# Optimization experiments

Measured on AMD Instinct MI355X. Metric: run time of the kernel, lower is better.

## Reference

```python
import jax, jax.numpy as jnp
import numpy as np

B, N, D, H = 4, 2048, 1024, 16
HD = D // H


def setup_inputs() -> dict:
    key = jax.random.key(0)
    ks = jax.random.split(key, 9)
    s = 1.0 / np.sqrt(D)
    return {
        "x": jax.random.normal(ks[0], (B, N, D), jnp.float32),
        "Wq": jax.random.normal(ks[1], (D, D), jnp.float32) * s,
        "bq": jnp.zeros((D,), jnp.float32),
        "Wk": jax.random.normal(ks[2], (D, D), jnp.float32) * s,
        "bk": jnp.zeros((D,), jnp.float32),
        "Wv": jax.random.normal(ks[3], (D, D), jnp.float32) * s,
        "bv": jnp.zeros((D,), jnp.float32),
        "Wo": jax.random.normal(ks[4], (D, D), jnp.float32) * s,
        "bo": jnp.zeros((D,), jnp.float32),
    }


def reference(x, Wq, bq, Wk, bk, Wv, bv, Wo, bo):
    Bx, Nx, Dx = x.shape
    q = x @ Wq + bq  # [B,N,D]
    k = x @ Wk + bk
    v = x @ Wv + bv
    # split heads -> [B,H,N,hd]
    q = q.reshape(Bx, Nx, H, HD).transpose(0, 2, 1, 3)
    k = k.reshape(Bx, Nx, H, HD).transpose(0, 2, 1, 3)
    v = v.reshape(Bx, Nx, H, HD).transpose(0, 2, 1, 3)
    q = q / jnp.sqrt(jnp.asarray(HD, q.dtype))
    scores = jnp.einsum("bhqd,bhkd->bhqk", q, k)
    # causal mask: additive -1e9 strictly above diagonal (matches torch.triu diag=1)
    mask = jnp.triu(jnp.full((Nx, Nx), -1e9, dtype=scores.dtype), k=1)
    probs = jax.nn.softmax(scores + mask, axis=-1)
    out = jnp.einsum("bhqk,bhkd->bhqd", probs, v)  # [B,H,N,hd]
    out = out.transpose(0, 2, 1, 3).reshape(Bx, Nx, Dx)  # concat heads
    return out @ Wo + bo
```

## Files before the change

### kernel.cpp

```cpp
#include <hip/hip_runtime.h>
#include <hip/hip_bf16.h>


#define BB 4
#define NN 2048
#define DD 1024
#define HH 16
#define HD 64
#define MM (BB * NN)

typedef __bf16 bf16;
typedef __bf16 bf16x8 __attribute__((ext_vector_type(8)));
typedef float f32x4 __attribute__((ext_vector_type(4)));

__device__ __forceinline__ void async_copy16(bf16* lds, const bf16* g) {
    __builtin_amdgcn_global_load_lds(
        (const __attribute__((address_space(1))) void*)g,
        (__attribute__((address_space(3))) void*)lds, 16, 0, 0);
}

__global__ void convert_x(const float* __restrict__ x, bf16* __restrict__ xb) {
    int i = (blockIdx.x * 256 + threadIdx.x) * 4;
    float4 v = *(const float4*)&x[i];
    xb[i + 0] = (bf16)v.x;
    xb[i + 1] = (bf16)v.y;
    xb[i + 2] = (bf16)v.z;
    xb[i + 3] = (bf16)v.w;
}

__global__ void transpose_w4(const float* __restrict__ W0, const float* __restrict__ W1,
                             const float* __restrict__ W2, const float* __restrict__ W3,
                             bf16* __restrict__ Wt) {
    __shared__ float tile[32][33];
    const float* W = (blockIdx.z == 0) ? W0 : (blockIdx.z == 1) ? W1
                    : (blockIdx.z == 2) ? W2 : W3;
    bf16* out = Wt + (size_t)blockIdx.z * DD * DD;
    int tx = threadIdx.x, ty = threadIdx.y;
    int x0 = blockIdx.x * 32, y0 = blockIdx.y * 32;
#pragma unroll
    for (int i = 0; i < 32; i += 8)
        tile[ty + i][tx] = W[(size_t)(y0 + ty + i) * DD + x0 + tx];
    __syncthreads();
#pragma unroll
    for (int i = 0; i < 32; i += 8)
        out[(size_t)(x0 + ty + i) * DD + y0 + tx] = (bf16)tile[tx][ty + i];
}

template <int MODE>
__global__ __launch_bounds__(256) void gemm_bt(
    const bf16* __restrict__ A, const bf16* __restrict__ Wt,
    const float* __restrict__ b0, const float* __restrict__ b1,
    const float* __restrict__ b2, void* __restrict__ out0,
    void* __restrict__ out1, void* __restrict__ out2) {
    const int K = DD;
    __shared__ __align__(16) bf16 As[128 * 32];
    __shared__ __align__(16) bf16 Bs[128 * 32];
    __shared__ __align__(16) bf16 Cs[MODE == 0 ? 128 * 136 : 1];

    int m0 = blockIdx.x * 128;
    int n0 = blockIdx.y * 128;

    const bf16* Wz;
    const float* bias;
    void* out;
    float scale = 1.0f;
    int z = 0;
    if (MODE == 0) {
        z = blockIdx.z;
        Wz = Wt + (size_t)z * DD * DD;
        bias = (z == 0) ? b0 : ((z == 1) ? b1 : b2);
        out = (z == 0) ? out0 : ((z == 1) ? out1 : out2);
        if (z == 0) scale = 0.125f * 1.44269504f;
    } else {
        Wz = Wt; bias = b0; out = out0;
    }

    int tid = threadIdx.x;
    int w = tid >> 6, lane = tid & 63;
    int wm = w >> 1, wn = w & 1;
    int quad = lane >> 4, l16 = lane & 15;

    f32x4 acc[4][4];
#pragma unroll
    for (int i = 0; i < 4; i++)
#pragma unroll
        for (int j = 0; j < 4; j++) acc[i][j] = (f32x4){0.f, 0.f, 0.f, 0.f};

    for (int k0 = 0; k0 < K; k0 += 32) {
        __syncthreads();
#pragma unroll
        for (int j = 0; j < 2; j++) {
            int c = j * 256 + w * 64 + lane;
            int row = c >> 2, kk = (c & 3) * 8;
            async_copy16(&As[c * 8], &A[(size_t)(m0 + row) * K + k0 + kk]);
            async_copy16(&Bs[c * 8], &Wz[(size_t)(n0 + row) * K + k0 + kk]);
        }
        __syncthreads();

        bf16x8 af[4], bfm[4];
#pragma unroll
        for (int i = 0; i < 4; i++) {
            af[i] = *(const bf16x8*)&As[(wm * 64 + i * 16 + l16) * 32 + quad * 8];
            bfm[i] = *(const bf16x8*)&Bs[(wn * 64 + i * 16 + l16) * 32 + quad * 8];
        }
#pragma unroll
        for (int i = 0; i < 4; i++)
#pragma unroll
            for (int j = 0; j < 4; j++)
                acc[i][j] = __builtin_amdgcn_mfma_f32_16x16x32_bf16(
                    af[i], bfm[j], acc[i][j], 0, 0, 0);
    }

    if (MODE == 0) {
#pragma unroll
        for (int j = 0; j < 4; j++) {
            int nl = wn * 64 + j * 16 + l16;
            float bv = bias[n0 + nl];
#pragma unroll
            for (int i = 0; i < 4; i++) {
#pragma unroll
                for (int r = 0; r < 4; r++) {
                    int ml = wm * 64 + i * 16 + quad * 4 + r;
                    bf16 v = (bf16)((acc[i][j][r] + bv) * scale);
                    if (z == 2) Cs[nl * 136 + ml] = v;
                    else        Cs[ml * 136 + nl] = v;
                }
            }
        }
        __syncthreads();

        int bidx = m0 >> 11;
        int tok0 = m0 & (NN - 1);
        int hh0 = n0 >> 6;
        if (z != 2) {
#pragma unroll
            for (int hf = 0; hf < 2; hf++) {
                bf16* base = (bf16*)out + ((size_t)(bidx * HH + hh0 + hf) * NN + tok0) * HD;
#pragma unroll
                for (int k = 0; k < 4; k++) {
                    int f = k * 2048 + tid * 8;
                    int tok = f >> 6, hd = f & 63;
                    *(bf16x8*)&base[f] = *(const bf16x8*)&Cs[tok * 136 + hf * 64 + hd];
                }
            }
        } else {
#pragma unroll
            for (int hf = 0; hf < 2; hf++) {
#pragma unroll
                for (int k = 0; k < 4; k++) {
                    int hd = k * 16 + (tid >> 4);
                    int tk = (tid & 15) * 8;
                    bf16* dst = (bf16*)out +
                        ((size_t)(bidx * HH + hh0 + hf) * HD + hd) * NN + tok0 + tk;
                    *(bf16x8*)dst = *(const bf16x8*)&Cs[(hf * 64 + hd) * 136 + tk];
                }
            }
        }
    } else {
#pragma unroll
        for (int j = 0; j < 4; j++) {
            int n = n0 + wn * 64 + j * 16 + l16;
            float bv = bias[n];
#pragma unroll
            for (int i = 0; i < 4; i++) {
                int mrow = m0 + wm * 64 + i * 16 + quad * 4;
#pragma unroll
                for (int r = 0; r < 4; r++)
                    ((float*)out)[(size_t)(mrow + r) * DD + n] = acc[i][j][r] + bv;
            }
        }
    }
}

__global__ __launch_bounds__(256) void flash_attn(
    const bf16* __restrict__ Q, const bf16* __restrict__ Kg,
    const bf16* __restrict__ Vt_g, bf16* __restrict__ Oc) {
    __shared__ __align__(16) bf16 Ks[128 * 72];
    __shared__ __align__(16) bf16 Vs[64 * 136];
    __shared__ __align__(16) bf16 Ps[128 * 136];

    int bh = blockIdx.y;
    int b = bh >> 4, h = bh & 15;
    int tid = threadIdx.x;
    int w = tid >> 6, lane = tid & 63;
    int quad = lane >> 4, l16 = lane & 15;

    const bf16* Qb = Q + (size_t)bh * NN * HD;
    const bf16* Kb = Kg + (size_t)bh * NN * HD;
    const bf16* Vtb = Vt_g + (size_t)bh * HD * NN;

    bf16x8 ones;
#pragma unroll
    for (int i = 0; i < 8; i++) ones[i] = (bf16)1.0f;

    int kr[4], kc[4], vd[4], vk[4];
#pragma unroll
    for (int j = 0; j < 4; j++) {
        int c = j * 256 + tid;
        kr[j] = c >> 3; kc[j] = (c & 7) * 8;
        vd[j] = c >> 4; vk[j] = (c & 15) * 8;
    }

    for (int phase = 0; phase < 2; phase++) {
        int qi = (phase == 0) ? blockIdx.x : (15 - blockIdx.x);
        int q0 = qi * 128;

        bf16x8 qf[2][2];
#pragma unroll
        for (int mi = 0; mi < 2; mi++)
#pragma unroll
            for (int ks = 0; ks < 2; ks++)
                qf[mi][ks] = *(const bf16x8*)&Qb[(size_t)(q0 + w * 32 + mi * 16 + l16) * HD +
                                                ks * 32 + quad * 8];

        f32x4 l_sum[2];
        f32x4 o_acc[2][4];
#pragma unroll
        for (int mi = 0; mi < 2; mi++) {
            l_sum[mi] = (f32x4){0.f, 0.f, 0.f, 0.f};
#pragma unroll
            for (int di = 0; di < 4; di++) o_acc[mi][di] = (f32x4){0.f, 0.f, 0.f, 0.f};
        }

        bf16x8 kreg[4], vreg[4];
#pragma unroll
        for (int j = 0; j < 4; j++) {
            kreg[j] = *(const bf16x8*)&Kb[(size_t)kr[j] * HD + kc[j]];
            vreg[j] = *(const bf16x8*)&Vtb[(size_t)vd[j] * NN + vk[j]];
        }

        for (int t = 0; t <= qi; t++) {
            __syncthreads();
#pragma unroll
            for (int j = 0; j < 4; j++) {
                *(bf16x8*)&Ks[kr[j] * 72 + kc[j]] = kreg[j];
                *(bf16x8*)&Vs[vd[j] * 136 + vk[j]] = vreg[j];
            }
            __syncthreads();

            if (t < qi) {
                int kvn = (t + 1) * 128;
#pragma unroll
                for (int j = 0; j < 4; j++) {
                    kreg[j] = *(const bf16x8*)&Kb[(size_t)(kvn + kr[j]) * HD + kc[j]];
                    vreg[j] = *(const bf16x8*)&Vtb[(size_t)vd[j] * NN + kvn + vk[j]];
                }
            }

            int kv0 = t * 128;
#pragma unroll
            for (int ni = 0; ni < 8; ni++) {
                bf16x8 bk0 = *(const bf16x8*)&Ks[(ni * 16 + l16) * 72 + quad * 8];
                bf16x8 bk1 = *(const bf16x8*)&Ks[(ni * 16 + l16) * 72 + 32 + quad * 8];
                f32x4 s0 = (f32x4){0.f, 0.f, 0.f, 0.f};
                f32x4 s1 = (f32x4){0.f, 0.f, 0.f, 0.f};
                s0 = __builtin_amdgcn_mfma_f32_16x16x32_bf16(qf[0][0], bk0, s0, 0, 0, 0);
                s0 = __builtin_amdgcn_mfma_f32_16x16x32_bf16(qf[0][1], bk1, s0, 0, 0, 0);
                s1 = __builtin_amdgcn_mfma_f32_16x16x32_bf16(qf[1][0], bk0, s1, 0, 0, 0);
                s1 = __builtin_amdgcn_mfma_f32_16x16x32_bf16(qf[1][1], bk1, s1, 0, 0, 0);
                int col = kv0 + ni * 16 + l16;
#pragma unroll
                for (int r = 0; r < 4; r++) {
                    int row0 = q0 + w * 32 + quad * 4 + r;
                    float p0 = (col > row0) ? 0.f : exp2f(s0[r]);
                    float p1 = (col > row0 + 16) ? 0.f : exp2f(s1[r]);
                    Ps[(w * 32 + quad * 4 + r) * 136 + ni * 16 + l16] = (bf16)p0;
                    Ps[(w * 32 + 16 + quad * 4 + r) * 136 + ni * 16 + l16] = (bf16)p1;
                }
            }

#pragma unroll
            for (int ks = 0; ks < 4; ks++) {
                bf16x8 pf0 = *(const bf16x8*)&Ps[(w * 32 + l16) * 136 + ks * 32 + quad * 8];
                bf16x8 pf1 = *(const bf16x8*)&Ps[(w * 32 + 16 + l16) * 136 + ks * 32 + quad * 8];
                l_sum[0] = __builtin_amdgcn_mfma_f32_16x16x32_bf16(pf0, ones, l_sum[0], 0, 0, 0);
                l_sum[1] = __builtin_amdgcn_mfma_f32_16x16x32_bf16(pf1, ones, l_sum[1], 0, 0, 0);
#pragma unroll
                for (int di = 0; di < 4; di++) {
                    bf16x8 bv = *(const bf16x8*)&Vs[(di * 16 + l16) * 136 + ks * 32 + quad * 8];
                    o_acc[0][di] = __builtin_amdgcn_mfma_f32_16x16x32_bf16(pf0, bv, o_acc[0][di], 0, 0, 0);
                    o_acc[1][di] = __builtin_amdgcn_mfma_f32_16x16x32_bf16(pf1, bv, o_acc[1][di], 0, 0, 0);
                }
            }
        }

#pragma unroll
        for (int mi = 0; mi < 2; mi++)
#pragma unroll
            for (int r = 0; r < 4; r++) {
                float inv = 1.0f / l_sum[mi][r];
                int tok = q0 + w * 32 + mi * 16 + quad * 4 + r;
#pragma unroll
                for (int di = 0; di < 4; di++) {
                    int d = h * 64 + di * 16 + l16;
                    Oc[((size_t)(b * NN + tok)) * DD + d] = (bf16)(o_acc[mi][di][r] * inv);
                }
            }
    }
}

extern "C" void kernel_launch(void* const* d_in, const int* in_sizes, int n_in,
                              void* d_out, int out_size, void* d_ws, size_t ws_size,
                              hipStream_t stream) {
    const float* x  = (const float*)d_in[0];
    const float* Wq = (const float*)d_in[1];
    const float* bq = (const float*)d_in[2];
    const float* Wk = (const float*)d_in[3];
    const float* bk = (const float*)d_in[4];
    const float* Wv = (const float*)d_in[5];
    const float* bv = (const float*)d_in[6];
    const float* Wo = (const float*)d_in[7];
    const float* bo = (const float*)d_in[8];

    const size_t need = (size_t)(8388608ull * 5 + 4194304ull) * sizeof(bf16);
    if (ws_size < need) return;

    bf16* ws = (bf16*)d_ws;
    bf16* xb = ws;
    bf16* wt = xb + (size_t)MM * DD;
    bf16* Qw = wt + 4ull * DD * DD;
    bf16* Kw = Qw + (size_t)MM * DD;
    bf16* Vw = Kw + (size_t)MM * DD;
    bf16* Aw = Vw + (size_t)MM * DD;

    convert_x<<<dim3(MM * DD / 1024), 256, 0, stream>>>(x, xb);

    transpose_w4<<<dim3(32, 32, 4), dim3(32, 8), 0, stream>>>(Wq, Wk, Wv, Wo, wt);

    gemm_bt<0><<<dim3(MM / 128, DD / 128, 3), 256, 0, stream>>>(
        xb, wt, bq, bk, bv, Qw, Kw, Vw);

    flash_attn<<<dim3(8, BB * HH), 256, 0, stream>>>(Qw, Kw, Vw, Aw);

    gemm_bt<1><<<dim3(MM / 128, DD / 128, 1), 256, 0, stream>>>(
        Aw, wt + 3ull * DD * DD, bo, bo, bo, d_out, d_out, d_out);
}
```

Measured before the change: 281.8 us.

## Split flash attention across 8 waves and compute scores transposed for vector stores

Each flash-attention block now runs 512 threads (8 waves of 16 query rows) instead of 256 (4 waves of 32 rows). This halves per-thread accumulators and K/V staging loads, which is meant to raise wave-level parallelism and occupancy. QK^T is computed with K as the A operand, so each lane holds 4 consecutive key columns and writes P to LDS as one bf16x4 store instead of scattered scalar stores. The causal mask is applied only on the diagonal tile. The grid is also reordered so batch-head varies fastest. The trade-off is more waves contending for the same LDS tiles and barriers.

After: 256.6 us. 1.1x faster.

```diff
diff --git a/kernel.cpp b/kernel.cpp
--- a/kernel.cpp
+++ b/kernel.cpp
@@ -10,6 +10,7 @@
 #define MM (BB * NN)
 
 typedef __bf16 bf16;
+typedef __bf16 bf16x4 __attribute__((ext_vector_type(4)));
 typedef __bf16 bf16x8 __attribute__((ext_vector_type(8)));
 typedef float f32x4 __attribute__((ext_vector_type(4)));
 
@@ -172,14 +173,14 @@
     }
 }
 
-__global__ __launch_bounds__(256) void flash_attn(
+__global__ __launch_bounds__(512, 4) void flash_attn(
     const bf16* __restrict__ Q, const bf16* __restrict__ Kg,
     const bf16* __restrict__ Vt_g, bf16* __restrict__ Oc) {
     __shared__ __align__(16) bf16 Ks[128 * 72];
     __shared__ __align__(16) bf16 Vs[64 * 136];
     __shared__ __align__(16) bf16 Ps[128 * 136];
 
-    int bh = blockIdx.y;
+    int bh = blockIdx.x;
     int b = bh >> 4, h = bh & 15;
     int tid = threadIdx.x;
     int w = tid >> 6, lane = tid & 63;
@@ -193,38 +194,34 @@
 #pragma unroll
     for (int i = 0; i < 8; i++) ones[i] = (bf16)1.0f;
 
-    int kr[4], kc[4], vd[4], vk[4];
-#pragma unroll
-    for (int j = 0; j < 4; j++) {
-        int c = j * 256 + tid;
+    int kr[2], kc[2], vd[2], vk[2];
+#pragma unroll
+    for (int j = 0; j < 2; j++) {
+        int c = j * 512 + tid;
         kr[j] = c >> 3; kc[j] = (c & 7) * 8;
         vd[j] = c >> 4; vk[j] = (c & 15) * 8;
     }
 
+    int psrow = (w * 16 + l16) * 136;
+
     for (int phase = 0; phase < 2; phase++) {
-        int qi = (phase == 0) ? blockIdx.x : (15 - blockIdx.x);
+        int qi = (phase == 0) ? blockIdx.y : (15 - blockIdx.y);
         int q0 = qi * 128;
-
-        bf16x8 qf[2][2];
-#pragma unroll
-        for (int mi = 0; mi < 2; mi++)
-#pragma unroll
-            for (int ks = 0; ks < 2; ks++)
-                qf[mi][ks] = *(const bf16x8*)&Qb[(size_t)(q0 + w * 32 + mi * 16 + l16) * HD +
-                                                ks * 32 + quad * 8];
-
-        f32x4 l_sum[2];
-        f32x4 o_acc[2][4];
-#pragma unroll
-        for (int mi = 0; mi < 2; mi++) {
-            l_sum[mi] = (f32x4){0.f, 0.f, 0.f, 0.f};
-#pragma unroll
-            for (int di = 0; di < 4; di++) o_acc[mi][di] = (f32x4){0.f, 0.f, 0.f, 0.f};
-        }
-
-        bf16x8 kreg[4], vreg[4];
-#pragma unroll
-        for (int j = 0; j < 4; j++) {
+        int qrow = q0 + w * 16 + l16;
+
+        bf16x8 qf[2];
+#pragma unroll
+        for (int ks = 0; ks < 2; ks++)
+            qf[ks] = *(const bf16x8*)&Qb[(size_t)qrow * HD + ks * 32 + quad * 8];
+
+        f32x4 l_sum = (f32x4){0.f, 0.f, 0.f, 0.f};
+        f32x4 o_acc[4];
+#pragma unroll
+        for (int di = 0; di < 4; di++) o_acc[di] = (f32x4){0.f, 0.f, 0.f, 0.f};
+
+        bf16x8 kreg[2], vreg[2];
+#pragma unroll
+        for (int j = 0; j < 2; j++) {
             kreg[j] = *(const bf16x8*)&Kb[(size_t)kr[j] * HD + kc[j]];
             vreg[j] = *(const bf16x8*)&Vtb[(size_t)vd[j] * NN + vk[j]];
         }
@@ -232,7 +229,7 @@
         for (int t = 0; t <= qi; t++) {
             __syncthreads();
 #pragma unroll
-            for (int j = 0; j < 4; j++) {
+            for (int j = 0; j < 2; j++) {
                 *(bf16x8*)&Ks[kr[j] * 72 + kc[j]] = kreg[j];
                 *(bf16x8*)&Vs[vd[j] * 136 + vk[j]] = vreg[j];
             }
@@ -241,61 +238,56 @@
             if (t < qi) {
                 int kvn = (t + 1) * 128;
 #pragma unroll
-                for (int j = 0; j < 4; j++) {
+                for (int j = 0; j < 2; j++) {
                     kreg[j] = *(const bf16x8*)&Kb[(size_t)(kvn + kr[j]) * HD + kc[j]];
                     vreg[j] = *(const bf16x8*)&Vtb[(size_t)vd[j] * NN + kvn + vk[j]];
                 }
             }
 
             int kv0 = t * 128;
+            bool diag = (t == qi);
 #pragma unroll
             for (int ni = 0; ni < 8; ni++) {
                 bf16x8 bk0 = *(const bf16x8*)&Ks[(ni * 16 + l16) * 72 + quad * 8];
                 bf16x8 bk1 = *(const bf16x8*)&Ks[(ni * 16 + l16) * 72 + 32 + quad * 8];
-                f32x4 s0 = (f32x4){0.f, 0.f, 0.f, 0.f};
-                f32x4 s1 = (f32x4){0.f, 0.f, 0.f, 0.f};
-                s0 = __builtin_amdgcn_mfma_f32_16x16x32_bf16(qf[0][0], bk0, s0, 0, 0, 0);
-                s0 = __builtin_amdgcn_mfma_f32_16x16x32_bf16(qf[0][1], bk1, s0, 0, 0, 0);
-                s1 = __builtin_amdgcn_mfma_f32_16x16x32_bf16(qf[1][0], bk0, s1, 0, 0, 0);
-                s1 = __builtin_amdgcn_mfma_f32_16x16x32_bf16(qf[1][1], bk1, s1, 0, 0, 0);
-                int col = kv0 + ni * 16 + l16;
-#pragma unroll
-                for (int r = 0; r < 4; r++) {
-                    int row0 = q0 + w * 32 + quad * 4 + r;
-                    float p0 = (col > row0) ? 0.f : exp2f(s0[r]);
-                    float p1 = (col > row0 + 16) ? 0.f : exp2f(s1[r]);
-                    Ps[(w * 32 + quad * 4 + r) * 136 + ni * 16 + l16] = (bf16)p0;
-                    Ps[(w * 32 + 16 + quad * 4 + r) * 136 + ni * 16 + l16] = (bf16)p1;
-                }
+                f32x4 s = (f32x4){0.f, 0.f, 0.f, 0.f};
+                s = __builtin_amdgcn_mfma_f32_16x16x32_bf16(bk0, qf[0], s, 0, 0, 0);
+                s = __builtin_amdgcn_mfma_f32_16x16x32_bf16(bk1, qf[1], s, 0, 0, 0);
+                bf16x4 pv;
+                if (diag) {
+                    int kvb = kv0 + ni * 16 + quad * 4;
+#pragma unroll
+                    for (int r = 0; r < 4; r++)
+                        pv[r] = (bf16)((kvb + r > qrow) ? 0.f : exp2f(s[r]));
+                } else {
+#pragma unroll
+                    for (int r = 0; r < 4; r++) pv[r] = (bf16)exp2f(s[r]);
+                }
+                *(bf16x4*)&Ps[psrow + ni * 16 + quad * 4] = pv;
             }
 
 #pragma unroll
             for (int ks = 0; ks < 4; ks++) {
-                bf16x8 pf0 = *(const bf16x8*)&Ps[(w * 32 + l16) * 136 + ks * 32 + quad * 8];
-                bf16x8 pf1 = *(const bf16x8*)&Ps[(w * 32 + 16 + l16) * 136 + ks * 32 + quad * 8];
-                l_sum[0] = __builtin_amdgcn_mfma_f32_16x16x32_bf16(pf0, ones, l_sum[0], 0, 0, 0);
-                l_sum[1] = __builtin_amdgcn_mfma_f32_16x16x32_bf16(pf1, ones, l_sum[1], 0, 0, 0);
+                bf16x8 pf = *(const bf16x8*)&Ps[psrow + ks * 32 + quad * 8];
+                l_sum = __builtin_amdgcn_mfma_f32_16x16x32_bf16(pf, ones, l_sum, 0, 0, 0);
 #pragma unroll
                 for (int di = 0; di < 4; di++) {
                     bf16x8 bv = *(const bf16x8*)&Vs[(di * 16 + l16) * 136 + ks * 32 + quad * 8];
-                    o_acc[0][di] = __builtin_amdgcn_mfma_f32_16x16x32_bf16(pf0, bv, o_acc[0][di], 0, 0, 0);
-                    o_acc[1][di] = __builtin_amdgcn_mfma_f32_16x16x32_bf16(pf1, bv, o_acc[1][di], 0, 0, 0);
-                }
-            }
-        }
-
-#pragma unroll
-        for (int mi = 0; mi < 2; mi++)
-#pragma unroll
-            for (int r = 0; r < 4; r++) {
-                float inv = 1.0f / l_sum[mi][r];
-                int tok = q0 + w * 32 + mi * 16 + quad * 4 + r;
-#pragma unroll
-                for (int di = 0; di < 4; di++) {
-                    int d = h * 64 + di * 16 + l16;
-                    Oc[((size_t)(b * NN + tok)) * DD + d] = (bf16)(o_acc[mi][di][r] * inv);
-                }
-            }
+                    o_acc[di] = __builtin_amdgcn_mfma_f32_16x16x32_bf16(pf, bv, o_acc[di], 0, 0, 0);
+                }
+            }
+        }
+
+#pragma unroll
+        for (int r = 0; r < 4; r++) {
+            float inv = 1.0f / l_sum[r];
+            int tok = q0 + w * 16 + quad * 4 + r;
+#pragma unroll
+            for (int di = 0; di < 4; di++) {
+                int d = h * 64 + di * 16 + l16;
+                Oc[((size_t)(b * NN + tok)) * DD + d] = (bf16)(o_acc[di][r] * inv);
+            }
+        }
     }
 }
 
@@ -330,7 +322,7 @@
     gemm_bt<0><<<dim3(MM / 128, DD / 128, 3), 256, 0, stream>>>(
         xb, wt, bq, bk, bv, Qw, Kw, Vw);
 
-    flash_attn<<<dim3(8, BB * HH), 256, 0, stream>>>(Qw, Kw, Vw, Aw);
+    flash_attn<<<dim3(BB * HH, 8), 512, 0, stream>>>(Qw, Kw, Vw, Aw);
 
     gemm_bt<1><<<dim3(MM / 128, DD / 128, 1), 256, 0, stream>>>(
         Aw, wt + 3ull * DD * DD, bo, bo, bo, d_out, d_out, d_out);
```
